# Performance work log

Hardware: AMD Instinct MI355X
Metric: run time of the kernel (lower is better)

The kernel has to match this reference:

```python
import jax, jax.numpy as jnp
import numpy as np

K = 6
EPS = 1e-7
BN_EPS = 1e-5


def tagconv(x, row, col, n, lins, bias, mw1, mb1, bng, bnb, mw2, mb2):
    # gcn_norm: symmetric normalization, no self-loops, edge_weight = 1
    deg = jax.ops.segment_sum(jnp.ones(row.shape[0], x.dtype), col, num_segments=n)
    dis = jnp.where(deg > 0, jax.lax.rsqrt(jnp.maximum(deg, 1.0)), 0.0)
    norm = dis[row] * dis[col]  # [E]
    out = x @ lins[0]
    h = x
    for k in range(1, K + 1):
        # message: relu(edge_weight * x_j) + eps, then scatter-add to destination
        msg = jax.nn.relu(norm[:, None] * h[row]) + EPS  # [E, C]
        h = jax.ops.segment_sum(msg, col, num_segments=n)
        out = out + h @ lins[k]
    out = out + bias
    # MLP: Linear -> BatchNorm1d(eval: running mean 0, var 1) -> ReLU -> Dropout(eval) -> Linear
    z = out @ mw1 + mb1
    z = bng * (z * (1.0 / np.sqrt(1.0 + BN_EPS))) + bnb
    z = jax.nn.relu(z)
    return z @ mw2 + mb2


def setup_inputs() -> dict:
    key = jax.random.key(0)
    ks = jax.random.split(key, 8)
    N, E, F, H, C = 50000, 800000, 128, 128, 64
    s = 0.05
    return {
        "x": jax.random.normal(ks[0], (N, F), jnp.float32),
        "edge_index": jax.random.randint(ks[1], (2, E), 0, N, jnp.int64),
        "lins1": jax.random.normal(ks[2], (K + 1, F, H), jnp.float32) * s,
        "bias1": jnp.zeros((H,), jnp.float32),
        "m1w1": jax.random.normal(ks[3], (H, 2 * H), jnp.float32) * s,
        "m1b1": jnp.zeros((2 * H,), jnp.float32),
        "bn1g": jnp.ones((2 * H,), jnp.float32),
        "bn1b": jnp.zeros((2 * H,), jnp.float32),
        "m1w2": jax.random.normal(ks[4], (2 * H, H), jnp.float32) * s,
        "m1b2": jnp.zeros((H,), jnp.float32),
        "lins2": jax.random.normal(ks[5], (K + 1, H, C), jnp.float32) * s,
        "bias2": jnp.zeros((C,), jnp.float32),
        "m2w1": jax.random.normal(ks[6], (C, 2 * C), jnp.float32) * s,
        "m2b1": jnp.zeros((2 * C,), jnp.float32),
        "bn2g": jnp.ones((2 * C,), jnp.float32),
        "bn2b": jnp.zeros((2 * C,), jnp.float32),
        "m2w2": jax.random.normal(ks[7], (2 * C, C), jnp.float32) * s,
        "m2b2": jnp.zeros((C,), jnp.float32),
    }


def reference(x, edge_index, lins1, bias1, m1w1, m1b1, bn1g, bn1b, m1w2, m1b2,
              lins2, bias2, m2w1, m2b1, bn2g, bn2b, m2w2, m2b2):
    n = x.shape[0]
    row, col = edge_index[0], edge_index[1]
    h = tagconv(x, row, col, n, lins1, bias1, m1w1, m1b1, bn1g, bn1b, m1w2, m1b2)
    h = jax.nn.relu(h)  # dropout is identity in eval mode
    return tagconv(h, row, col, n, lins2, bias2, m2w1, m2b1, bn2g, bn2b, m2w2, m2b2)
```

## Files before the change

kernel.cpp:

```cpp
#include <hip/hip_runtime.h>
#include <hip/hip_bf16.h>


#define EPS_MSG 1e-7f
#define BNSCALE 0.9999950000374997f
#define LO_INV 0.0009765625f

typedef _Float16 half_t;
typedef _Float16 f16x8 __attribute__((ext_vector_type(8)));
typedef float f32x4 __attribute__((ext_vector_type(4)));

__device__ __forceinline__ void gld16(const char* g, char* l) {
    __builtin_amdgcn_global_load_lds(
        (const __attribute__((address_space(1))) void*)g,
        (__attribute__((address_space(3))) void*)l, 16, 0, 0);
}

__device__ __forceinline__ float hlo(unsigned p) {
    unsigned short u = (unsigned short)(p & 0xffffu);
    half_t h;
    __builtin_memcpy(&h, &u, 2);
    return (float)h;
}
__device__ __forceinline__ float hhi(unsigned p) {
    unsigned short u = (unsigned short)(p >> 16);
    half_t h;
    __builtin_memcpy(&h, &u, 2);
    return (float)h;
}
__device__ __forceinline__ unsigned fpack2(float x, float y) {
    half_t a = (half_t)x, b = (half_t)y;
    unsigned short ua, ub;
    __builtin_memcpy(&ua, &a, 2);
    __builtin_memcpy(&ub, &b, 2);
    return (unsigned)ua | ((unsigned)ub << 16);
}

__device__ __forceinline__ float epi_apply(float v, int gc, int epi,
                                           const float* __restrict__ bias,
                                           const float* __restrict__ bng,
                                           const float* __restrict__ bnb) {
    if (epi == 1) {
        v += bias[gc];
    } else if (epi == 2) {
        v = bng[gc] * ((v + bias[gc]) * BNSCALE) + bnb[gc];
        v = fmaxf(v, 0.f);
    } else if (epi == 3) {
        v = fmaxf(v + bias[gc], 0.f);
    }
    return v;
}


__global__ void zero_i32(int* __restrict__ p, int n) {
    int i = blockIdx.x * blockDim.x + threadIdx.x;
    if (i < n) p[i] = 0;
}

__global__ void count_deg(const int* __restrict__ col, int* __restrict__ deg, int E) {
    int e = blockIdx.x * blockDim.x + threadIdx.x;
    if (e < E) atomicAdd(&deg[col[e]], 1);
}

__global__ void compute_dis_s(const int* __restrict__ deg, float* __restrict__ dis,
                              float* __restrict__ s, float* __restrict__ rs, int N) {
    int v = blockIdx.x * blockDim.x + threadIdx.x;
    if (v >= N) return;
    int d = deg[v];
    float di = (d > 0) ? rsqrtf((float)d) : 0.f;
    dis[v] = di;
    s[v] = (d > 0) ? di : 1.f;
    rs[v] = (d > 0) ? sqrtf((float)d) : 1.f;
}

__global__ void scan_blk(const int* __restrict__ deg, int* __restrict__ off,
                         int* __restrict__ bsum, int N) {
    __shared__ int sm[1024];
    int i = blockIdx.x * 1024 + threadIdx.x;
    sm[threadIdx.x] = (i < N) ? deg[i] : 0;
    __syncthreads();
    for (int ofs = 1; ofs < 1024; ofs <<= 1) {
        int t = (threadIdx.x >= (unsigned)ofs) ? sm[threadIdx.x - ofs] : 0;
        __syncthreads();
        sm[threadIdx.x] += t;
        __syncthreads();
    }
    if (i < N) off[i + 1] = sm[threadIdx.x];
    if (threadIdx.x == 0) bsum[blockIdx.x] = sm[1023];
}

__global__ void scan_top(int* __restrict__ bsum, int nb) {
    if (threadIdx.x == 0 && blockIdx.x == 0) {
        int a = 0;
        for (int b = 0; b < nb; ++b) {
            int t = bsum[b];
            bsum[b] = a;
            a += t;
        }
    }
}

__global__ void scan_add(int* __restrict__ off, const int* __restrict__ bsum, int N) {
    int i = blockIdx.x * 1024 + threadIdx.x;
    if (i < N) off[i + 1] += bsum[blockIdx.x];
    if (i == 0) off[0] = 0;
}

__global__ void fill_edges(const int* __restrict__ row, const int* __restrict__ col,
                           const int* __restrict__ off, int* __restrict__ cur,
                           unsigned short* __restrict__ esrc, int E) {
    int e = blockIdx.x * blockDim.x + threadIdx.x;
    if (e >= E) return;
    int c = col[e];
    int pos = off[c] + atomicAdd(&cur[c], 1);
    esrc[pos] = (unsigned short)row[e];
}


__global__ void conv_xg(const float* __restrict__ x, half_t* __restrict__ slab,
                        half_t* __restrict__ g0, const float* __restrict__ dis,
                        const float* __restrict__ s, int total) {
    int i = blockIdx.x * blockDim.x + threadIdx.x;
    if (i >= total) return;
    int v = i >> 7, c = i & 127;
    float xv = x[i];
    slab[(size_t)v * 896 + c] = (half_t)(s[v] * xv);
    g0[i] = (half_t)(dis[v] * fmaxf(xv, 0.f));
}

__device__ __forceinline__ void wcv(const float* __restrict__ in, half_t* __restrict__ oh,
                                    half_t* __restrict__ ol, int nm, int K, int Nn, int i) {
    int KT = nm * K;
    int n = i / KT;
    int rem = i - n * KT;
    int km = rem / K, k = rem - km * K;
    float w = in[(size_t)km * K * Nn + (size_t)k * Nn + n];
    half_t h = (half_t)w;
    oh[i] = h;
    ol[i] = (half_t)((w - (float)h) * 1024.f);
}

__global__ void conv_all(const float* l1, const float* l2, const float* a1, const float* b1,
                         const float* a2, const float* b2, half_t* W1h, half_t* W1l,
                         half_t* W2h, half_t* W2l, half_t* M1ah, half_t* M1al, half_t* M1bh,
                         half_t* M1bl, half_t* M2ah, half_t* M2al, half_t* M2bh,
                         half_t* M2bl) {
    int i = blockIdx.x * blockDim.x + threadIdx.x;
    if (i < 114688) {
        wcv(l1, W1h, W1l, 7, 128, 128, i);
    } else if (i < 172032) {
        int j = i - 114688;
        int np = j >> 7, k = j & 127;
        int km = np >> 6, n = np & 63;
        float w = l2[(size_t)km * 128 * 64 + (size_t)k * 64 + n];
        half_t h = (half_t)w;
        W2h[j] = h;
        W2l[j] = (half_t)((w - (float)h) * 1024.f);
    } else if (i < 204800) {
        wcv(a1, M1ah, M1al, 1, 128, 256, i - 172032);
    } else if (i < 237568) {
        wcv(b1, M1bh, M1bl, 1, 256, 128, i - 204800);
    } else if (i < 245760) {
        wcv(a2, M2ah, M2al, 1, 64, 128, i - 237568);
    } else if (i < 253952) {
        wcv(b2, M2bh, M2bl, 1, 128, 64, i - 245760);
    }
}

__global__ void trows_part(const float* __restrict__ l2, float* __restrict__ partial) {
    __shared__ float sm[256];
    int k = blockIdx.x / 8 + 1;
    int p = blockIdx.x % 8;
    int c = threadIdx.x & 63;
    int q = threadIdx.x >> 6;
    float a = 0.f;
    int kk0 = p * 16 + q * 4;
#pragma unroll
    for (int t = 0; t < 4; ++t)
        a += l2[(size_t)k * 128 * 64 + (kk0 + t) * 64 + c];
    sm[threadIdx.x] = a;
    __syncthreads();
    if (q == 0)
        partial[(size_t)blockIdx.x * 64 + c] =
            (sm[c] + sm[64 + c]) + (sm[128 + c] + sm[192 + c]);
}

__global__ void trows_final(const float* __restrict__ partial, float* __restrict__ T) {
    int j = threadIdx.x >> 6;
    int c = threadIdx.x & 63;
    if (j >= 6) return;
    float a = 0.f;
    for (int k = j + 1; k <= 6; ++k)
#pragma unroll
        for (int p = 0; p < 8; ++p) a += partial[(size_t)((k - 1) * 8 + p) * 64 + c];
    T[j * 64 + c] = a;
}


__global__ void __launch_bounds__(256) prop(const unsigned* __restrict__ gin, int idl,
                                            unsigned* __restrict__ gout, int odl,
                                            const float* __restrict__ dis,
                                            const int* __restrict__ off,
                                            const unsigned short* __restrict__ esrc, int N) {
    const int lane = threadIdx.x & 63;
    const int w = threadIdx.x >> 6;
    const int stride = gridDim.x * 4;
    for (int v = blockIdx.x * 4 + w; v < N; v += stride) {
        int s = off[v], e = off[v + 1];
        float2 A0 = {0.f, 0.f}, A1 = {0.f, 0.f}, A2 = {0.f, 0.f}, A3 = {0.f, 0.f};
        float2 A4 = {0.f, 0.f}, A5 = {0.f, 0.f}, A6 = {0.f, 0.f}, A7 = {0.f, 0.f};
        for (int i = s; i < e; i += 8) {
            unsigned p[8];
            int ok[8];
#pragma unroll
            for (int j = 0; j < 8; ++j) {
                int ij = i + j;
                ok[j] = ij < e;
                int idx = ok[j] ? ij : e - 1;
                p[j] = gin[esrc[idx] * idl + lane];
            }
            A0.x += ok[0] ? hlo(p[0]) : 0.f; A0.y += ok[0] ? hhi(p[0]) : 0.f;
            A1.x += ok[1] ? hlo(p[1]) : 0.f; A1.y += ok[1] ? hhi(p[1]) : 0.f;
            A2.x += ok[2] ? hlo(p[2]) : 0.f; A2.y += ok[2] ? hhi(p[2]) : 0.f;
            A3.x += ok[3] ? hlo(p[3]) : 0.f; A3.y += ok[3] ? hhi(p[3]) : 0.f;
            A4.x += ok[4] ? hlo(p[4]) : 0.f; A4.y += ok[4] ? hhi(p[4]) : 0.f;
            A5.x += ok[5] ? hlo(p[5]) : 0.f; A5.y += ok[5] ? hhi(p[5]) : 0.f;
            A6.x += ok[6] ? hlo(p[6]) : 0.f; A6.y += ok[6] ? hhi(p[6]) : 0.f;
            A7.x += ok[7] ? hlo(p[7]) : 0.f; A7.y += ok[7] ? hhi(p[7]) : 0.f;
        }
        float ax = ((A0.x + A1.x) + (A2.x + A3.x)) + ((A4.x + A5.x) + (A6.x + A7.x));
        float ay = ((A0.y + A1.y) + (A2.y + A3.y)) + ((A4.y + A5.y) + (A6.y + A7.y));
        float dv = dis[v];
        float ce = (float)(e - s) * EPS_MSG;
        float hx = fmaf(dv, ax, ce);
        float hy = fmaf(dv, ay, ce);
        gout[v * odl + lane] = fpack2(dv * hx, dv * hy);
    }
}


template <int FINAL>
__global__ void __launch_bounds__(256) prop64(
    const half_t* __restrict__ uin, int ldu, const half_t* __restrict__ pj, int ldp,
    half_t* __restrict__ uout, int ldo, const float* __restrict__ dis,
    const int* __restrict__ off, const unsigned short* __restrict__ esrc,
    const float* __restrict__ tj, const float* __restrict__ bias2, int N) {
    const int c = threadIdx.x & 63;
    const int w = threadIdx.x >> 6;
    const int stride = gridDim.x * 4;
    for (int v = blockIdx.x * 4 + w; v < N; v += stride) {
        int s = off[v], e = off[v + 1];
        float a0 = 0.f, a1 = 0.f, a2 = 0.f, a3 = 0.f;
        float a4 = 0.f, a5 = 0.f, a6 = 0.f, a7 = 0.f;
        for (int i = s; i < e; i += 8) {
            float q[8];
            int ok[8];
#pragma unroll
            for (int j = 0; j < 8; ++j) {
                int ij = i + j;
                ok[j] = ij < e;
                int idx = ok[j] ? ij : e - 1;
                q[j] = (float)uin[(size_t)esrc[idx] * ldu + c];
            }
            a0 += ok[0] ? q[0] : 0.f;
            a1 += ok[1] ? q[1] : 0.f;
            a2 += ok[2] ? q[2] : 0.f;
            a3 += ok[3] ? q[3] : 0.f;
            a4 += ok[4] ? q[4] : 0.f;
            a5 += ok[5] ? q[5] : 0.f;
            a6 += ok[6] ? q[6] : 0.f;
            a7 += ok[7] ? q[7] : 0.f;
        }
        float acc = ((a0 + a1) + (a2 + a3)) + ((a4 + a5) + (a6 + a7));
        float dv = dis[v];
        float base = (float)pj[(size_t)v * ldp + c] + (float)(e - s) * EPS_MSG * tj[c];
        float u = fmaf(dv, acc, base);
        if (FINAL)
            uout[(size_t)v * ldo + c] = (half_t)(u + bias2[c]);
        else
            uout[(size_t)v * ldo + c] = (half_t)(dv * u);
    }
}


__global__ __launch_bounds__(512) void gemmc(
    int M, int kiters, const half_t* __restrict__ A, int lda,
    const half_t* __restrict__ Bhp, const half_t* __restrict__ Blp, int ldb,
    half_t* __restrict__ Cp, int ldc, const float* __restrict__ rs,
    const float* __restrict__ bias) {
    constexpr int ABY = 8192, BBY = 8192, BUFBY = ABY + 2 * BBY;
    __shared__ __align__(16) char lds[2][BUFBY];

    const int tid = threadIdx.x, lane = tid & 63, w = tid >> 6;
    const int wr = w >> 1, wc = w & 1;
    const int m0 = blockIdx.x * 128;
    const int l15 = lane & 15, lq = lane >> 4;
    const int lr = lane >> 2, lc = lane & 3;

    const char* gA = (const char*)A;
    const char* gBh = (const char*)Bhp;
    const char* gBl = (const char*)Blp;
    const size_t ldaB = (size_t)lda * 2, ldbB = (size_t)ldb * 2;

    auto stage = [&](int kt, int buf) {
        const int k0b = kt * 64;
        char* base = lds[0] + buf * BUFBY;
        int r = w * 16 + lr;
        int sc = (lc ^ (r & 3)) << 4;
        {
            int gv = m0 + r;
            if (gv >= M) gv = M - 1;
            gld16(gA + (size_t)gv * ldaB + k0b + sc, base + w * 1024);
        }
        {
            size_t goff = (size_t)r * ldbB + k0b + sc;
            gld16(gBh + goff, base + ABY + w * 1024);
            gld16(gBl + goff, base + ABY + BBY + w * 1024);
        }
    };

    f32x4 acch[2][4], accl[2][4];
#pragma unroll
    for (int fm = 0; fm < 2; ++fm)
#pragma unroll
        for (int fn = 0; fn < 4; ++fn) {
            acch[fm][fn] = (f32x4){0.f, 0.f, 0.f, 0.f};
            accl[fm][fn] = (f32x4){0.f, 0.f, 0.f, 0.f};
        }

    auto compute = [&](int buf) {
        const char* Ab = lds[0] + buf * BUFBY;
        const char* Bhb = Ab + ABY;
        const char* Blb = Ab + ABY + BBY;
        f16x8 af[2];
#pragma unroll
        for (int fm = 0; fm < 2; ++fm) {
            int ra = wr * 32 + fm * 16 + l15;
            af[fm] = *(const f16x8*)(Ab + ra * 64 + ((lq ^ (ra & 3)) << 4));
        }
#pragma unroll
        for (int fn = 0; fn < 4; ++fn) {
            int rb = wc * 64 + fn * 16 + l15;
            int o = rb * 64 + ((lq ^ (rb & 3)) << 4);
            f16x8 bhv = *(const f16x8*)(Bhb + o);
            f16x8 blv = *(const f16x8*)(Blb + o);
#pragma unroll
            for (int fm = 0; fm < 2; ++fm) {
                acch[fm][fn] = __builtin_amdgcn_mfma_f32_16x16x32_f16(af[fm], bhv, acch[fm][fn], 0, 0, 0);
                accl[fm][fn] = __builtin_amdgcn_mfma_f32_16x16x32_f16(af[fm], blv, accl[fm][fn], 0, 0, 0);
            }
        }
    };

    stage(0, 0);
    int buf = 0;
    for (int kt = 0; kt < kiters; ++kt) {
        __syncthreads();
        if (kt + 1 < kiters) stage(kt + 1, buf ^ 1);
        compute(buf);
        buf ^= 1;
    }

#pragma unroll
    for (int fm = 0; fm < 2; ++fm)
#pragma unroll
        for (int fn = 0; fn < 4; ++fn)
#pragma unroll
            for (int i = 0; i < 4; ++i) {
                int gr = m0 + wr * 32 + fm * 16 + lq * 4 + i;
                if (gr >= M) continue;
                int gc = wc * 64 + fn * 16 + l15;
                float v = acch[fm][fn][i] + accl[fm][fn][i] * LO_INV;
                v = v * rs[gr] + bias[gc];
                Cp[(size_t)gr * ldc + gc] = (half_t)v;
            }
}


template <int KT, int NS, int OUTF32>
__global__ __launch_bounds__(256) void gemmn(
    int M, const half_t* __restrict__ A, int lda, const half_t* __restrict__ Bhp,
    const half_t* __restrict__ Blp, int ldb, void* __restrict__ Cp, int ldc, int epi,
    const float* __restrict__ bias, const float* __restrict__ bng,
    const float* __restrict__ bnb, const float* __restrict__ scaleRows, int scaleStrip) {
    constexpr int KI = KT / 32;
    constexpr int T = NS * KI;
    constexpr int CPR = KT / 8;
    constexpr int LPR = CPR;
    constexpr int RPC = 64 / LPR;
    constexpr int SW = (CPR < 16) ? CPR - 1 : 15;
    constexpr int ACH = (64 * KT * 2) / 1024;
    constexpr int ACW = ACH / 4;
    constexpr int ABY = 64 * KT * 2;
    constexpr int BPB = 4096;
    __shared__ __align__(16) char lds[ABY + 4 * BPB];

    const int tid = threadIdx.x, lane = tid & 63, w = tid >> 6;
    const int m0 = blockIdx.x * 64;
    const int l15 = lane & 15, lq = lane >> 4;
    const int lr = lane >> 2, lc = lane & 3;

    const char* gA = (const char*)A;
    const char* gBh = (const char*)Bhp;
    const char* gBl = (const char*)Blp;
    const size_t ldaB = (size_t)lda * 2, ldbB = (size_t)ldb * 2;

#pragma unroll
    for (int i = 0; i < ACW; ++i) {
        int c = w * ACW + i;
        int r = c * RPC + lane / LPR;
        int col = lane % LPR;
        int scol = col ^ (r & SW);
        int gv = m0 + r;
        if (gv >= M) gv = M - 1;
        gld16(gA + (size_t)gv * ldaB + scol * 16, lds + c * 1024);
    }

    auto stageB = [&](int ns, int kt, int buf) {
        char* bb = lds + ABY + buf * 2 * BPB;
        int r = w * 16 + lr;
        int sc = (lc ^ (r & 3)) << 4;
        size_t goff = (size_t)(ns * 64 + r) * ldbB + kt * 64 + sc;
        gld16(gBh + goff, bb + w * 1024);
        gld16(gBl + goff, bb + BPB + w * 1024);
    };

    f32x4 acch[4], accl[4];

    auto compute = [&](int buf, int kt) {
        const char* Ab = lds;
        const char* Bhb = lds + ABY + buf * 2 * BPB;
        const char* Blb = Bhb + BPB;
        int ra = w * 16 + l15;
        int cc = kt * 4 + lq;
        f16x8 af = *(const f16x8*)(Ab + ra * (KT * 2) + ((cc ^ (ra & SW)) << 4));
#pragma unroll
        for (int fn = 0; fn < 4; ++fn) {
            int rb = fn * 16 + l15;
            int o = rb * 64 + ((lq ^ (rb & 3)) << 4);
            f16x8 bhv = *(const f16x8*)(Bhb + o);
            f16x8 blv = *(const f16x8*)(Blb + o);
            acch[fn] = __builtin_amdgcn_mfma_f32_16x16x32_f16(af, bhv, acch[fn], 0, 0, 0);
            accl[fn] = __builtin_amdgcn_mfma_f32_16x16x32_f16(af, blv, accl[fn], 0, 0, 0);
        }
    };

    stageB(0, 0, 0);
    int buf = 0;
    for (int t = 0; t < T; ++t) {
        int ns = t / KI, kt = t - ns * KI;
        __syncthreads();
        if (t + 1 < T) {
            int t1 = t + 1;
            stageB(t1 / KI, t1 - (t1 / KI) * KI, buf ^ 1);
        }
        if (kt == 0) {
#pragma unroll
            for (int fn = 0; fn < 4; ++fn) {
                acch[fn] = (f32x4){0.f, 0.f, 0.f, 0.f};
                accl[fn] = (f32x4){0.f, 0.f, 0.f, 0.f};
            }
        }
        compute(buf, kt);
        if (kt == KI - 1) {
#pragma unroll
            for (int fn = 0; fn < 4; ++fn)
#pragma unroll
                for (int i = 0; i < 4; ++i) {
                    int gr = m0 + w * 16 + lq * 4 + i;
                    if (gr >= M) continue;
                    int gc = ns * 64 + fn * 16 + l15;
                    float v = acch[fn][i] + accl[fn][i] * LO_INV;
                    if (ns == scaleStrip) v *= scaleRows[gr];
                    v = epi_apply(v, gc, epi, bias, bng, bnb);
                    if (OUTF32)
                        ((float*)Cp)[(size_t)gr * ldc + gc] = v;
                    else
                        ((half_t*)Cp)[(size_t)gr * ldc + gc] = (half_t)v;
                }
        }
        buf ^= 1;
    }
}

extern "C" void kernel_launch(void* const* d_in, const int* in_sizes, int n_in,
                              void* d_out, int out_size, void* d_ws, size_t ws_size,
                              hipStream_t stream) {
    const float* x     = (const float*)d_in[0];
    const int*   ei    = (const int*)d_in[1];
    const float* lins1 = (const float*)d_in[2];
    const float* bias1 = (const float*)d_in[3];
    const float* m1w1  = (const float*)d_in[4];
    const float* m1b1  = (const float*)d_in[5];
    const float* bn1g  = (const float*)d_in[6];
    const float* bn1b  = (const float*)d_in[7];
    const float* m1w2  = (const float*)d_in[8];
    const float* m1b2  = (const float*)d_in[9];
    const float* lins2 = (const float*)d_in[10];
    const float* bias2 = (const float*)d_in[11];
    const float* m2w1  = (const float*)d_in[12];
    const float* m2b1  = (const float*)d_in[13];
    const float* bn2g  = (const float*)d_in[14];
    const float* bn2b  = (const float*)d_in[15];
    const float* m2w2  = (const float*)d_in[16];
    const float* m2b2  = (const float*)d_in[17];
    float* out = (float*)d_out;

    const int N = in_sizes[0] / 128;
    const int E = in_sizes[1] / 2;
    const int* row = ei;
    const int* col = ei + E;

    char* ws = (char*)d_ws;
    size_t o = 0;
    auto alloc = [&](size_t bytes) {
        void* p = ws + o;
        o += (bytes + 255) & ~(size_t)255;
        return p;
    };
    int*            deg  = (int*)alloc((size_t)N * 4);
    int*            cur  = (int*)alloc((size_t)N * 4);
    float*          dis  = (float*)alloc((size_t)N * 4);
    float*          sA   = (float*)alloc((size_t)N * 4);
    float*          rsA  = (float*)alloc((size_t)N * 4);
    int*            off  = (int*)alloc((size_t)(N + 1) * 4);
    int*            bsum = (int*)alloc(1024 * 4);
    float*          Trow = (float*)alloc(6 * 64 * 4);
    float*          Tpar = (float*)alloc(48 * 64 * 4);
    unsigned short* esrc = (unsigned short*)alloc((size_t)E * 2);
    half_t* g0    = (half_t*)alloc((size_t)N * 128 * 2);
    half_t* ACC   = (half_t*)alloc((size_t)N * 128 * 2);
    half_t* Z     = (half_t*)alloc((size_t)N * 256 * 2);
    half_t* H1    = (half_t*)alloc((size_t)N * 128 * 2);
    half_t* ACC2  = (half_t*)alloc((size_t)N * 64 * 2);
    half_t* Wc1h  = (half_t*)alloc((size_t)128 * 896 * 2);
    half_t* Wc1l  = (half_t*)alloc((size_t)128 * 896 * 2);
    half_t* Wc2h  = (half_t*)alloc((size_t)448 * 128 * 2);
    half_t* Wc2l  = (half_t*)alloc((size_t)448 * 128 * 2);
    half_t* Wm1ah = (half_t*)alloc((size_t)256 * 128 * 2);
    half_t* Wm1al = (half_t*)alloc((size_t)256 * 128 * 2);
    half_t* Wm1bh = (half_t*)alloc((size_t)128 * 256 * 2);
    half_t* Wm1bl = (half_t*)alloc((size_t)128 * 256 * 2);
    half_t* Wm2ah = (half_t*)alloc((size_t)128 * 64 * 2);
    half_t* Wm2al = (half_t*)alloc((size_t)128 * 64 * 2);
    half_t* Wm2bh = (half_t*)alloc((size_t)64 * 128 * 2);
    half_t* Wm2bl = (half_t*)alloc((size_t)64 * 128 * 2);
    half_t* slab  = (half_t*)alloc((size_t)N * 896 * 2);
    (void)ws_size;

    const int TPB = 256;
    const int nb = (N + 1023) / 1024;
    zero_i32<<<(N + TPB - 1) / TPB, TPB, 0, stream>>>(deg, N);
    zero_i32<<<(N + TPB - 1) / TPB, TPB, 0, stream>>>(cur, N);
    count_deg<<<(E + TPB - 1) / TPB, TPB, 0, stream>>>(col, deg, E);
    compute_dis_s<<<(N + TPB - 1) / TPB, TPB, 0, stream>>>(deg, dis, sA, rsA, N);
    scan_blk<<<nb, 1024, 0, stream>>>(deg, off, bsum, N);
    scan_top<<<1, 64, 0, stream>>>(bsum, nb);
    scan_add<<<nb, 1024, 0, stream>>>(off, bsum, N);
    fill_edges<<<(E + TPB - 1) / TPB, TPB, 0, stream>>>(row, col, off, cur, esrc, E);
    conv_all<<<(253952 + TPB - 1) / TPB, TPB, 0, stream>>>(
        lins1, lins2, m1w1, m1w2, m2w1, m2w2, Wc1h, Wc1l, Wc2h, Wc2l, Wm1ah, Wm1al, Wm1bh,
        Wm1bl, Wm2ah, Wm2al, Wm2bh, Wm2bl);
    trows_part<<<48, 256, 0, stream>>>(lins2, Tpar);
    trows_final<<<1, 384, 0, stream>>>(Tpar, Trow);
    conv_xg<<<(N * 128 + TPB - 1) / TPB, TPB, 0, stream>>>(x, slab, g0, dis, sA, N * 128);

    unsigned* slabU = (unsigned*)slab;
    unsigned* g0U = (unsigned*)g0;
    const int HG = (N + 63) / 64;
    const int HG128 = (N + 127) / 128;

    prop<<<2048, 256, 0, stream>>>(g0U, 64, slabU + 64, 448, dis, off, esrc, N);
    for (int k = 2; k <= 6; ++k)
        prop<<<2048, 256, 0, stream>>>(slabU + (size_t)(k - 1) * 64, 448,
                                       slabU + (size_t)k * 64, 448, dis, off, esrc, N);
    gemmc<<<HG128, 512, 0, stream>>>(N, 28, slab, 896, Wc1h, Wc1l, 896, ACC, 128, rsA, bias1);
    gemmn<128, 4, 0><<<HG, 256, 0, stream>>>(
        N, ACC, 128, Wm1ah, Wm1al, 128, Z, 256, 2, m1b1, bn1g, bn1b, nullptr, -1);
    gemmn<256, 2, 0><<<HG, 256, 0, stream>>>(
        N, Z, 256, Wm1bh, Wm1bl, 256, H1, 128, 3, m1b2, nullptr, nullptr, nullptr, -1);

    gemmn<128, 7, 0><<<HG, 256, 0, stream>>>(
        N, H1, 128, Wc2h, Wc2l, 128, slab, 448, 0, nullptr, nullptr, nullptr, dis, 6);

    half_t* ub0 = g0;
    half_t* ub1 = g0 + (size_t)N * 64;
    prop64<0><<<2048, 256, 0, stream>>>(slab + 384, 448, slab + 320, 448, ub0, 64, dis, off,
                                        esrc, Trow + 5 * 64, nullptr, N);
    prop64<0><<<2048, 256, 0, stream>>>(ub0, 64, slab + 256, 448, ub1, 64, dis, off, esrc,
                                        Trow + 4 * 64, nullptr, N);
    prop64<0><<<2048, 256, 0, stream>>>(ub1, 64, slab + 192, 448, ub0, 64, dis, off, esrc,
                                        Trow + 3 * 64, nullptr, N);
    prop64<0><<<2048, 256, 0, stream>>>(ub0, 64, slab + 128, 448, ub1, 64, dis, off, esrc,
                                        Trow + 2 * 64, nullptr, N);
    prop64<0><<<2048, 256, 0, stream>>>(ub1, 64, slab + 64, 448, ub0, 64, dis, off, esrc,
                                        Trow + 1 * 64, nullptr, N);
    prop64<1><<<2048, 256, 0, stream>>>(ub0, 64, slab, 448, ACC2, 64, dis, off, esrc,
                                        Trow + 0 * 64, bias2, N);

    gemmn<64, 2, 0><<<HG, 256, 0, stream>>>(
        N, ACC2, 64, Wm2ah, Wm2al, 64, Z, 128, 2, m2b1, bn2g, bn2b, nullptr, -1);
    gemmn<128, 1, 1><<<HG, 256, 0, stream>>>(
        N, Z, 128, Wm2bh, Wm2bl, 128, out, 64, 1, m2b2, nullptr, nullptr, nullptr, -1);
}
```

Measured before the change: 673.3 us.

## Fuse MLP GEMM chains into single kernels keeping intermediates in LDS

Merges the three back-to-back GEMMs after the first conv (MLP linear+BN+ReLU, second linear+ReLU, and the projection by lins2) into one kernel, and likewise the two MLP GEMMs at the end. Intermediate activations (Z, H1) live in shared memory instead of round-tripping through global memory, and several launches are dropped. It also merges the two zeroing kernels into one. In exchange, the larger per-block LDS footprint (about 64KB for fuse1) may lower occupancy and limit latency hiding.

Result: no change. 674.9 us (+0.2%).

```diff
diff --git a/kernel.cpp b/kernel.cpp
--- a/kernel.cpp
+++ b/kernel.cpp
@@ -36,25 +36,13 @@
     return (unsigned)ua | ((unsigned)ub << 16);
 }
 
-__device__ __forceinline__ float epi_apply(float v, int gc, int epi,
-                                           const float* __restrict__ bias,
-                                           const float* __restrict__ bng,
-                                           const float* __restrict__ bnb) {
-    if (epi == 1) {
-        v += bias[gc];
-    } else if (epi == 2) {
-        v = bng[gc] * ((v + bias[gc]) * BNSCALE) + bnb[gc];
-        v = fmaxf(v, 0.f);
-    } else if (epi == 3) {
-        v = fmaxf(v + bias[gc], 0.f);
-    }
-    return v;
-}
-
-
-__global__ void zero_i32(int* __restrict__ p, int n) {
+
+__global__ void zero2_i32(int* __restrict__ a, int* __restrict__ b, int n) {
     int i = blockIdx.x * blockDim.x + threadIdx.x;
-    if (i < n) p[i] = 0;
+    if (i < n) {
+        a[i] = 0;
+        b[i] = 0;
+    }
 }
 
 __global__ void count_deg(const int* __restrict__ col, int* __restrict__ deg, int E) {
@@ -377,63 +365,70 @@
 }
 
 
-template <int KT, int NS, int OUTF32>
-__global__ __launch_bounds__(256) void gemmn(
-    int M, const half_t* __restrict__ A, int lda, const half_t* __restrict__ Bhp,
-    const half_t* __restrict__ Blp, int ldb, void* __restrict__ Cp, int ldc, int epi,
-    const float* __restrict__ bias, const float* __restrict__ bng,
-    const float* __restrict__ bnb, const float* __restrict__ scaleRows, int scaleStrip) {
-    constexpr int KI = KT / 32;
-    constexpr int T = NS * KI;
-    constexpr int CPR = KT / 8;
-    constexpr int LPR = CPR;
-    constexpr int RPC = 64 / LPR;
-    constexpr int SW = (CPR < 16) ? CPR - 1 : 15;
-    constexpr int ACH = (64 * KT * 2) / 1024;
-    constexpr int ACW = ACH / 4;
-    constexpr int ABY = 64 * KT * 2;
+__global__ __launch_bounds__(256) void fuse1(
+    int M, const half_t* __restrict__ ACC, const half_t* __restrict__ W1h,
+    const half_t* __restrict__ W1l, const half_t* __restrict__ W2h,
+    const half_t* __restrict__ W2l, const half_t* __restrict__ WPh,
+    const half_t* __restrict__ WPl, half_t* __restrict__ P, int ldp,
+    const float* __restrict__ b1, const float* __restrict__ bg,
+    const float* __restrict__ bb, const float* __restrict__ b2,
+    const float* __restrict__ disArr) {
     constexpr int BPB = 4096;
-    __shared__ __align__(16) char lds[ABY + 4 * BPB];
+    __shared__ __align__(16) char ldsA[16384];
+    __shared__ __align__(16) char ldsZ[32768];
+    __shared__ __align__(16) char ldsB[4 * BPB];
 
     const int tid = threadIdx.x, lane = tid & 63, w = tid >> 6;
     const int m0 = blockIdx.x * 64;
     const int l15 = lane & 15, lq = lane >> 4;
     const int lr = lane >> 2, lc = lane & 3;
 
-    const char* gA = (const char*)A;
-    const char* gBh = (const char*)Bhp;
-    const char* gBl = (const char*)Blp;
-    const size_t ldaB = (size_t)lda * 2, ldbB = (size_t)ldb * 2;
-
-#pragma unroll
-    for (int i = 0; i < ACW; ++i) {
-        int c = w * ACW + i;
-        int r = c * RPC + lane / LPR;
-        int col = lane % LPR;
-        int scol = col ^ (r & SW);
+#pragma unroll
+    for (int i = 0; i < 4; ++i) {
+        int c = w * 4 + i;
+        int r = c * 4 + (lane >> 4);
+        int colx = lane & 15;
+        int scol = colx ^ (r & 15);
         int gv = m0 + r;
         if (gv >= M) gv = M - 1;
-        gld16(gA + (size_t)gv * ldaB + scol * 16, lds + c * 1024);
-    }
-
-    auto stageB = [&](int ns, int kt, int buf) {
-        char* bb = lds + ABY + buf * 2 * BPB;
+        gld16((const char*)ACC + (size_t)gv * 256 + scol * 16, ldsA + c * 1024);
+    }
+
+    auto stageB = [&](const char* Bh_, const char* Bl_, size_t ldbB_, int rowoff, int kt,
+                      int bufb) {
+        char* bbuf = ldsB + bufb * 2 * BPB;
         int r = w * 16 + lr;
         int sc = (lc ^ (r & 3)) << 4;
-        size_t goff = (size_t)(ns * 64 + r) * ldbB + kt * 64 + sc;
-        gld16(gBh + goff, bb + w * 1024);
-        gld16(gBl + goff, bb + BPB + w * 1024);
+        size_t goff = (size_t)(rowoff + r) * ldbB_ + (size_t)kt * 64 + sc;
+        gld16(Bh_ + goff, bbuf + w * 1024);
+        gld16(Bl_ + goff, bbuf + BPB + w * 1024);
+    };
+    auto stageTile = [&](int t, int bufb) {
+        if (t < 16) {
+            stageB((const char*)W1h, (const char*)W1l, 256, (t >> 2) * 64, t & 3, bufb);
+        } else if (t < 32) {
+            int tt = t - 16;
+            stageB((const char*)W2h, (const char*)W2l, 512, (tt >> 3) * 64, tt & 7, bufb);
+        } else {
+            int tt = t - 32;
+            stageB((const char*)WPh, (const char*)WPl, 256, (tt >> 2) * 64, tt & 3, bufb);
+        }
     };
 
     f32x4 acch[4], accl[4];
-
-    auto compute = [&](int buf, int kt) {
-        const char* Ab = lds;
-        const char* Bhb = lds + ABY + buf * 2 * BPB;
+    auto zacc = [&]() {
+#pragma unroll
+        for (int fn = 0; fn < 4; ++fn) {
+            acch[fn] = (f32x4){0.f, 0.f, 0.f, 0.f};
+            accl[fn] = (f32x4){0.f, 0.f, 0.f, 0.f};
+        }
+    };
+    auto computeT = [&](const char* Ab, int astride, int asw, int bufb, int cc0) {
+        const char* Bhb = ldsB + bufb * 2 * BPB;
         const char* Blb = Bhb + BPB;
         int ra = w * 16 + l15;
-        int cc = kt * 4 + lq;
-        f16x8 af = *(const f16x8*)(Ab + ra * (KT * 2) + ((cc ^ (ra & SW)) << 4));
+        int cc = cc0 + lq;
+        f16x8 af = *(const f16x8*)(Ab + ra * astride + ((cc ^ (ra & asw)) << 4));
 #pragma unroll
         for (int fn = 0; fn < 4; ++fn) {
             int rb = fn * 16 + l15;
@@ -445,39 +440,176 @@
         }
     };
 
-    stageB(0, 0, 0);
+    stageTile(0, 0);
     int buf = 0;
-    for (int t = 0; t < T; ++t) {
-        int ns = t / KI, kt = t - ns * KI;
+    for (int t = 0; t < 60; ++t) {
         __syncthreads();
-        if (t + 1 < T) {
-            int t1 = t + 1;
-            stageB(t1 / KI, t1 - (t1 / KI) * KI, buf ^ 1);
-        }
-        if (kt == 0) {
-#pragma unroll
-            for (int fn = 0; fn < 4; ++fn) {
-                acch[fn] = (f32x4){0.f, 0.f, 0.f, 0.f};
-                accl[fn] = (f32x4){0.f, 0.f, 0.f, 0.f};
-            }
-        }
-        compute(buf, kt);
-        if (kt == KI - 1) {
-#pragma unroll
-            for (int fn = 0; fn < 4; ++fn)
-#pragma unroll
-                for (int i = 0; i < 4; ++i) {
-                    int gr = m0 + w * 16 + lq * 4 + i;
-                    if (gr >= M) continue;
-                    int gc = ns * 64 + fn * 16 + l15;
-                    float v = acch[fn][i] + accl[fn][i] * LO_INV;
-                    if (ns == scaleStrip) v *= scaleRows[gr];
-                    v = epi_apply(v, gc, epi, bias, bng, bnb);
-                    if (OUTF32)
-                        ((float*)Cp)[(size_t)gr * ldc + gc] = v;
-                    else
-                        ((half_t*)Cp)[(size_t)gr * ldc + gc] = (half_t)v;
-                }
+        if (t + 1 < 60) stageTile(t + 1, buf ^ 1);
+        if (t < 16) {
+            int kt = t & 3, ns = t >> 2;
+            if (kt == 0) zacc();
+            computeT(ldsA, 256, 15, buf, kt * 4);
+            if (kt == 3) {
+#pragma unroll
+                for (int fn = 0; fn < 4; ++fn)
+#pragma unroll
+                    for (int i = 0; i < 4; ++i) {
+                        int r = w * 16 + lq * 4 + i;
+                        int gc = ns * 64 + fn * 16 + l15;
+                        float v = acch[fn][i] + accl[fn][i] * LO_INV;
+                        v = bg[gc] * ((v + b1[gc]) * BNSCALE) + bb[gc];
+                        v = fmaxf(v, 0.f);
+                        int ch = (gc >> 3) ^ (r & 15);
+                        *(half_t*)(ldsZ + r * 512 + (ch << 4) + (gc & 7) * 2) = (half_t)v;
+                    }
+            }
+        } else if (t < 32) {
+            int tt = t - 16, kt = tt & 7, ns = tt >> 3;
+            if (kt == 0) zacc();
+            computeT(ldsZ, 512, 15, buf, kt * 4);
+            if (kt == 7) {
+#pragma unroll
+                for (int fn = 0; fn < 4; ++fn)
+#pragma unroll
+                    for (int i = 0; i < 4; ++i) {
+                        int r = w * 16 + lq * 4 + i;
+                        int gc = ns * 64 + fn * 16 + l15;
+                        float v = acch[fn][i] + accl[fn][i] * LO_INV;
+                        v = fmaxf(v + b2[gc], 0.f);
+                        int ch = (gc >> 3) ^ (r & 15);
+                        *(half_t*)(ldsA + r * 256 + (ch << 4) + (gc & 7) * 2) = (half_t)v;
+                    }
+            }
+        } else {
+            int tt = t - 32, kt = tt & 3, ns = tt >> 2;
+            if (kt == 0) zacc();
+            computeT(ldsA, 256, 15, buf, kt * 4);
+            if (kt == 3) {
+#pragma unroll
+                for (int fn = 0; fn < 4; ++fn)
+#pragma unroll
+                    for (int i = 0; i < 4; ++i) {
+                        int gr = m0 + w * 16 + lq * 4 + i;
+                        if (gr >= M) continue;
+                        int gc = ns * 64 + fn * 16 + l15;
+                        float v = acch[fn][i] + accl[fn][i] * LO_INV;
+                        if (ns == 6) v *= disArr[gr];
+                        P[(size_t)gr * ldp + gc] = (half_t)v;
+                    }
+            }
+        }
+        buf ^= 1;
+    }
+}
+
+
+__global__ __launch_bounds__(256) void fuse2(
+    int M, const half_t* __restrict__ ACC2, const half_t* __restrict__ W1h,
+    const half_t* __restrict__ W1l, const half_t* __restrict__ W2h,
+    const half_t* __restrict__ W2l, float* __restrict__ outp,
+    const float* __restrict__ b1, const float* __restrict__ bg,
+    const float* __restrict__ bb, const float* __restrict__ b2) {
+    constexpr int BPB = 4096;
+    __shared__ __align__(16) char ldsA[8192];
+    __shared__ __align__(16) char ldsZ[16384];
+    __shared__ __align__(16) char ldsB[4 * BPB];
+
+    const int tid = threadIdx.x, lane = tid & 63, w = tid >> 6;
+    const int m0 = blockIdx.x * 64;
+    const int l15 = lane & 15, lq = lane >> 4;
+    const int lr = lane >> 2, lc = lane & 3;
+
+#pragma unroll
+    for (int i = 0; i < 2; ++i) {
+        int c = w * 2 + i;
+        int r = c * 8 + (lane >> 3);
+        int colx = lane & 7;
+        int scol = colx ^ (r & 7);
+        int gv = m0 + r;
+        if (gv >= M) gv = M - 1;
+        gld16((const char*)ACC2 + (size_t)gv * 128 + scol * 16, ldsA + c * 1024);
+    }
+
+    auto stageB = [&](const char* Bh_, const char* Bl_, size_t ldbB_, int rowoff, int kt,
+                      int bufb) {
+        char* bbuf = ldsB + bufb * 2 * BPB;
+        int r = w * 16 + lr;
+        int sc = (lc ^ (r & 3)) << 4;
+        size_t goff = (size_t)(rowoff + r) * ldbB_ + (size_t)kt * 64 + sc;
+        gld16(Bh_ + goff, bbuf + w * 1024);
+        gld16(Bl_ + goff, bbuf + BPB + w * 1024);
+    };
+    auto stageTile = [&](int t, int bufb) {
+        if (t < 4)
+            stageB((const char*)W1h, (const char*)W1l, 128, (t >> 1) * 64, t & 1, bufb);
+        else
+            stageB((const char*)W2h, (const char*)W2l, 256, 0, t - 4, bufb);
+    };
+
+    f32x4 acch[4], accl[4];
+    auto zacc = [&]() {
+#pragma unroll
+        for (int fn = 0; fn < 4; ++fn) {
+            acch[fn] = (f32x4){0.f, 0.f, 0.f, 0.f};
+            accl[fn] = (f32x4){0.f, 0.f, 0.f, 0.f};
+        }
+    };
+    auto computeT = [&](const char* Ab, int astride, int asw, int bufb, int cc0) {
+        const char* Bhb = ldsB + bufb * 2 * BPB;
+        const char* Blb = Bhb + BPB;
+        int ra = w * 16 + l15;
+        int cc = cc0 + lq;
+        f16x8 af = *(const f16x8*)(Ab + ra * astride + ((cc ^ (ra & asw)) << 4));
+#pragma unroll
+        for (int fn = 0; fn < 4; ++fn) {
+            int rb = fn * 16 + l15;
+            int o = rb * 64 + ((lq ^ (rb & 3)) << 4);
+            f16x8 bhv = *(const f16x8*)(Bhb + o);
+            f16x8 blv = *(const f16x8*)(Blb + o);
+            acch[fn] = __builtin_amdgcn_mfma_f32_16x16x32_f16(af, bhv, acch[fn], 0, 0, 0);
+            accl[fn] = __builtin_amdgcn_mfma_f32_16x16x32_f16(af, blv, accl[fn], 0, 0, 0);
+        }
+    };
+
+    stageTile(0, 0);
+    int buf = 0;
+    for (int t = 0; t < 8; ++t) {
+        __syncthreads();
+        if (t + 1 < 8) stageTile(t + 1, buf ^ 1);
+        if (t < 4) {
+            int kt = t & 1, ns = t >> 1;
+            if (kt == 0) zacc();
+            computeT(ldsA, 128, 7, buf, kt * 4);
+            if (kt == 1) {
+#pragma unroll
+                for (int fn = 0; fn < 4; ++fn)
+#pragma unroll
+                    for (int i = 0; i < 4; ++i) {
+                        int r = w * 16 + lq * 4 + i;
+                        int gc = ns * 64 + fn * 16 + l15;
+                        float v = acch[fn][i] + accl[fn][i] * LO_INV;
+                        v = bg[gc] * ((v + b1[gc]) * BNSCALE) + bb[gc];
+                        v = fmaxf(v, 0.f);
+                        int ch = (gc >> 3) ^ (r & 15);
+                        *(half_t*)(ldsZ + r * 256 + (ch << 4) + (gc & 7) * 2) = (half_t)v;
+                    }
+            }
+        } else {
+            int tt = t - 4;
+            if (tt == 0) zacc();
+            computeT(ldsZ, 256, 15, buf, tt * 4);
+            if (tt == 3) {
+#pragma unroll
+                for (int fn = 0; fn < 4; ++fn)
+#pragma unroll
+                    for (int i = 0; i < 4; ++i) {
+                        int gr = m0 + w * 16 + lq * 4 + i;
+                        if (gr >= M) continue;
+                        int gc = fn * 16 + l15;
+                        float v = acch[fn][i] + accl[fn][i] * LO_INV;
+                        outp[(size_t)gr * 64 + gc] = v + b2[gc];
+                    }
+            }
         }
         buf ^= 1;
     }
@@ -530,8 +662,6 @@
     unsigned short* esrc = (unsigned short*)alloc((size_t)E * 2);
     half_t* g0    = (half_t*)alloc((size_t)N * 128 * 2);
     half_t* ACC   = (half_t*)alloc((size_t)N * 128 * 2);
-    half_t* Z     = (half_t*)alloc((size_t)N * 256 * 2);
-    half_t* H1    = (half_t*)alloc((size_t)N * 128 * 2);
     half_t* ACC2  = (half_t*)alloc((size_t)N * 64 * 2);
     half_t* Wc1h  = (half_t*)alloc((size_t)128 * 896 * 2);
     half_t* Wc1l  = (half_t*)alloc((size_t)128 * 896 * 2);
@@ -550,8 +680,7 @@
 
     const int TPB = 256;
     const int nb = (N + 1023) / 1024;
-    zero_i32<<<(N + TPB - 1) / TPB, TPB, 0, stream>>>(deg, N);
-    zero_i32<<<(N + TPB - 1) / TPB, TPB, 0, stream>>>(cur, N);
+    zero2_i32<<<(N + TPB - 1) / TPB, TPB, 0, stream>>>(deg, cur, N);
     count_deg<<<(E + TPB - 1) / TPB, TPB, 0, stream>>>(col, deg, E);
     compute_dis_s<<<(N + TPB - 1) / TPB, TPB, 0, stream>>>(deg, dis, sA, rsA, N);
     scan_blk<<<nb, 1024, 0, stream>>>(deg, off, bsum, N);
@@ -575,13 +704,9 @@
         prop<<<2048, 256, 0, stream>>>(slabU + (size_t)(k - 1) * 64, 448,
                                        slabU + (size_t)k * 64, 448, dis, off, esrc, N);
     gemmc<<<HG128, 512, 0, stream>>>(N, 28, slab, 896, Wc1h, Wc1l, 896, ACC, 128, rsA, bias1);
-    gemmn<128, 4, 0><<<HG, 256, 0, stream>>>(
-        N, ACC, 128, Wm1ah, Wm1al, 128, Z, 256, 2, m1b1, bn1g, bn1b, nullptr, -1);
-    gemmn<256, 2, 0><<<HG, 256, 0, stream>>>(
-        N, Z, 256, Wm1bh, Wm1bl, 256, H1, 128, 3, m1b2, nullptr, nullptr, nullptr, -1);
-
-    gemmn<128, 7, 0><<<HG, 256, 0, stream>>>(
-        N, H1, 128, Wc2h, Wc2l, 128, slab, 448, 0, nullptr, nullptr, nullptr, dis, 6);
+
+    fuse1<<<HG, 256, 0, stream>>>(N, ACC, Wm1ah, Wm1al, Wm1bh, Wm1bl, Wc2h, Wc2l, slab, 448,
+                                  m1b1, bn1g, bn1b, m1b2, dis);
 
     half_t* ub0 = g0;
     half_t* ub1 = g0 + (size_t)N * 64;
@@ -598,8 +723,6 @@
     prop64<1><<<2048, 256, 0, stream>>>(ub0, 64, slab, 448, ACC2, 64, dis, off, esrc,
                                         Trow + 0 * 64, bias2, N);
 
-    gemmn<64, 2, 0><<<HG, 256, 0, stream>>>(
-        N, ACC2, 64, Wm2ah, Wm2al, 64, Z, 128, 2, m2b1, bn2g, bn2b, nullptr, -1);
-    gemmn<128, 1, 1><<<HG, 256, 0, stream>>>(
-        N, Z, 128, Wm2bh, Wm2bl, 128, out, 64, 1, m2b2, nullptr, nullptr, nullptr, -1);
-}
+    fuse2<<<HG, 256, 0, stream>>>(N, ACC2, Wm2ah, Wm2al, Wm2bh, Wm2bl, out, m2b1, bn2g, bn2b,
+                                  m2b2);
+}
```

## Merge propagation hops into cooperative kernels and fuse final MLP GEMMs

Applied to the files above, without the earlier changes.

Replaces the six layer-1 propagation launches and the six Horner propagation launches with two cooperative kernels that step through the hops using grid-wide syncs. It also fuses the final two MLP GEMMs into one kernel that keeps the hidden activations in LDS, and merges the two zeroing kernels into one. The intent is to cut launch overhead and the round trip of the Z intermediate through global memory. In exchange the cooperative grid is limited to 1024 blocks, down from 2048, which may reduce latency hiding in the gather loops, and each grid.sync adds barrier cost.

Result: slower. 1.992 ms (+195.8%).

```diff
diff --git a/kernel.cpp b/kernel.cpp
--- a/kernel.cpp
+++ b/kernel.cpp
@@ -1,5 +1,6 @@
 #include <hip/hip_runtime.h>
 #include <hip/hip_bf16.h>
+#include <hip/hip_cooperative_groups.h>
 
 
 #define EPS_MSG 1e-7f
@@ -9,6 +10,8 @@
 typedef _Float16 half_t;
 typedef _Float16 f16x8 __attribute__((ext_vector_type(8)));
 typedef float f32x4 __attribute__((ext_vector_type(4)));
+
+namespace cg = cooperative_groups;
 
 __device__ __forceinline__ void gld16(const char* g, char* l) {
     __builtin_amdgcn_global_load_lds(
@@ -52,9 +55,12 @@
 }
 
 
-__global__ void zero_i32(int* __restrict__ p, int n) {
+__global__ void zero2_i32(int* __restrict__ a, int* __restrict__ b, int n) {
     int i = blockIdx.x * blockDim.x + threadIdx.x;
-    if (i < n) p[i] = 0;
+    if (i < n) {
+        a[i] = 0;
+        b[i] = 0;
+    }
 }
 
 __global__ void count_deg(const int* __restrict__ col, int* __restrict__ deg, int E) {
@@ -197,11 +203,11 @@
 }
 
 
-__global__ void __launch_bounds__(256) prop(const unsigned* __restrict__ gin, int idl,
-                                            unsigned* __restrict__ gout, int odl,
-                                            const float* __restrict__ dis,
-                                            const int* __restrict__ off,
-                                            const unsigned short* __restrict__ esrc, int N) {
+__device__ __forceinline__ void prop_hop(const unsigned* __restrict__ gin, int idl,
+                                         unsigned* __restrict__ gout, int odl,
+                                         const float* __restrict__ dis,
+                                         const int* __restrict__ off,
+                                         const unsigned short* __restrict__ esrc, int N) {
     const int lane = threadIdx.x & 63;
     const int w = threadIdx.x >> 6;
     const int stride = gridDim.x * 4;
@@ -238,13 +244,29 @@
     }
 }
 
-
-template <int FINAL>
-__global__ void __launch_bounds__(256) prop64(
-    const half_t* __restrict__ uin, int ldu, const half_t* __restrict__ pj, int ldp,
-    half_t* __restrict__ uout, int ldo, const float* __restrict__ dis,
-    const int* __restrict__ off, const unsigned short* __restrict__ esrc,
-    const float* __restrict__ tj, const float* __restrict__ bias2, int N) {
+__global__ void __launch_bounds__(256) prop6(const unsigned* __restrict__ g0U,
+                                             unsigned* __restrict__ slabU,
+                                             const float* __restrict__ dis,
+                                             const int* __restrict__ off,
+                                             const unsigned short* __restrict__ esrc, int N) {
+    cg::grid_group grid = cg::this_grid();
+    prop_hop(g0U, 64, slabU + 64, 448, dis, off, esrc, N);
+    for (int k = 2; k <= 6; ++k) {
+        grid.sync();
+        prop_hop(slabU + (size_t)(k - 1) * 64, 448, slabU + (size_t)k * 64, 448, dis, off,
+                 esrc, N);
+    }
+}
+
+__device__ __forceinline__ void horner_step(const half_t* __restrict__ uin, int ldu,
+                                            const half_t* __restrict__ pj,
+                                            half_t* __restrict__ uout,
+                                            const float* __restrict__ dis,
+                                            const int* __restrict__ off,
+                                            const unsigned short* __restrict__ esrc,
+                                            const float* __restrict__ tj,
+                                            const float* __restrict__ bias2, int finalStep,
+                                            int N) {
     const int c = threadIdx.x & 63;
     const int w = threadIdx.x >> 6;
     const int stride = gridDim.x * 4;
@@ -273,13 +295,36 @@
         }
         float acc = ((a0 + a1) + (a2 + a3)) + ((a4 + a5) + (a6 + a7));
         float dv = dis[v];
-        float base = (float)pj[(size_t)v * ldp + c] + (float)(e - s) * EPS_MSG * tj[c];
+        float base = (float)pj[(size_t)v * 448 + c] + (float)(e - s) * EPS_MSG * tj[c];
         float u = fmaf(dv, acc, base);
-        if (FINAL)
-            uout[(size_t)v * ldo + c] = (half_t)(u + bias2[c]);
+        if (finalStep)
+            uout[(size_t)v * 64 + c] = (half_t)(u + bias2[c]);
         else
-            uout[(size_t)v * ldo + c] = (half_t)(dv * u);
-    }
+            uout[(size_t)v * 64 + c] = (half_t)(dv * u);
+    }
+}
+
+__global__ void __launch_bounds__(256) horner6(const half_t* __restrict__ slab,
+                                               half_t* __restrict__ ub0,
+                                               half_t* __restrict__ ub1,
+                                               half_t* __restrict__ ACC2,
+                                               const float* __restrict__ dis,
+                                               const int* __restrict__ off,
+                                               const unsigned short* __restrict__ esrc,
+                                               const float* __restrict__ Trow,
+                                               const float* __restrict__ bias2, int N) {
+    cg::grid_group grid = cg::this_grid();
+    horner_step(slab + 384, 448, slab + 320, ub0, dis, off, esrc, Trow + 5 * 64, nullptr, 0, N);
+    grid.sync();
+    horner_step(ub0, 64, slab + 256, ub1, dis, off, esrc, Trow + 4 * 64, nullptr, 0, N);
+    grid.sync();
+    horner_step(ub1, 64, slab + 192, ub0, dis, off, esrc, Trow + 3 * 64, nullptr, 0, N);
+    grid.sync();
+    horner_step(ub0, 64, slab + 128, ub1, dis, off, esrc, Trow + 2 * 64, nullptr, 0, N);
+    grid.sync();
+    horner_step(ub1, 64, slab + 64, ub0, dis, off, esrc, Trow + 1 * 64, nullptr, 0, N);
+    grid.sync();
+    horner_step(ub0, 64, slab, ACC2, dis, off, esrc, Trow, bias2, 1, N);
 }
 
 
@@ -478,6 +523,119 @@
                     else
                         ((half_t*)Cp)[(size_t)gr * ldc + gc] = (half_t)v;
                 }
+        }
+        buf ^= 1;
+    }
+}
+
+
+__global__ __launch_bounds__(256) void fuse2(
+    int M, const half_t* __restrict__ ACC2, const half_t* __restrict__ W1h,
+    const half_t* __restrict__ W1l, const half_t* __restrict__ W2h,
+    const half_t* __restrict__ W2l, float* __restrict__ outp,
+    const float* __restrict__ b1, const float* __restrict__ bg,
+    const float* __restrict__ bb, const float* __restrict__ b2) {
+    constexpr int BPB = 4096;
+    __shared__ __align__(16) char ldsA[8192];
+    __shared__ __align__(16) char ldsZ[16384];
+    __shared__ __align__(16) char ldsB[4 * BPB];
+
+    const int tid = threadIdx.x, lane = tid & 63, w = tid >> 6;
+    const int m0 = blockIdx.x * 64;
+    const int l15 = lane & 15, lq = lane >> 4;
+    const int lr = lane >> 2, lc = lane & 3;
+
+#pragma unroll
+    for (int i = 0; i < 2; ++i) {
+        int c = w * 2 + i;
+        int r = c * 8 + (lane >> 3);
+        int colx = lane & 7;
+        int scol = colx ^ (r & 7);
+        int gv = m0 + r;
+        if (gv >= M) gv = M - 1;
+        gld16((const char*)ACC2 + (size_t)gv * 128 + scol * 16, ldsA + c * 1024);
+    }
+
+    auto stageB = [&](const char* Bh_, const char* Bl_, size_t ldbB_, int rowoff, int kt,
+                      int bufb) {
+        char* bbuf = ldsB + bufb * 2 * BPB;
+        int r = w * 16 + lr;
+        int sc = (lc ^ (r & 3)) << 4;
+        size_t goff = (size_t)(rowoff + r) * ldbB_ + (size_t)kt * 64 + sc;
+        gld16(Bh_ + goff, bbuf + w * 1024);
+        gld16(Bl_ + goff, bbuf + BPB + w * 1024);
+    };
+    auto stageTile = [&](int t, int bufb) {
+        if (t < 4)
+            stageB((const char*)W1h, (const char*)W1l, 128, (t >> 1) * 64, t & 1, bufb);
+        else
+            stageB((const char*)W2h, (const char*)W2l, 256, 0, t - 4, bufb);
+    };
+
+    f32x4 acch[4], accl[4];
+    auto zacc = [&]() {
+#pragma unroll
+        for (int fn = 0; fn < 4; ++fn) {
+            acch[fn] = (f32x4){0.f, 0.f, 0.f, 0.f};
+            accl[fn] = (f32x4){0.f, 0.f, 0.f, 0.f};
+        }
+    };
+    auto computeT = [&](const char* Ab, int astride, int asw, int bufb, int cc0) {
+        const char* Bhb = ldsB + bufb * 2 * BPB;
+        const char* Blb = Bhb + BPB;
+        int ra = w * 16 + l15;
+        int cc = cc0 + lq;
+        f16x8 af = *(const f16x8*)(Ab + ra * astride + ((cc ^ (ra & asw)) << 4));
+#pragma unroll
+        for (int fn = 0; fn < 4; ++fn) {
+            int rb = fn * 16 + l15;
+            int o = rb * 64 + ((lq ^ (rb & 3)) << 4);
+            f16x8 bhv = *(const f16x8*)(Bhb + o);
+            f16x8 blv = *(const f16x8*)(Blb + o);
+            acch[fn] = __builtin_amdgcn_mfma_f32_16x16x32_f16(af, bhv, acch[fn], 0, 0, 0);
+            accl[fn] = __builtin_amdgcn_mfma_f32_16x16x32_f16(af, blv, accl[fn], 0, 0, 0);
+        }
+    };
+
+    stageTile(0, 0);
+    int buf = 0;
+    for (int t = 0; t < 8; ++t) {
+        __syncthreads();
+        if (t + 1 < 8) stageTile(t + 1, buf ^ 1);
+        if (t < 4) {
+            int kt = t & 1, ns = t >> 1;
+            if (kt == 0) zacc();
+            computeT(ldsA, 128, 7, buf, kt * 4);
+            if (kt == 1) {
+#pragma unroll
+                for (int fn = 0; fn < 4; ++fn)
+#pragma unroll
+                    for (int i = 0; i < 4; ++i) {
+                        int r = w * 16 + lq * 4 + i;
+                        int gc = ns * 64 + fn * 16 + l15;
+                        float v = acch[fn][i] + accl[fn][i] * LO_INV;
+                        v = bg[gc] * ((v + b1[gc]) * BNSCALE) + bb[gc];
+                        v = fmaxf(v, 0.f);
+                        int ch = (gc >> 3) ^ (r & 15);
+                        *(half_t*)(ldsZ + r * 256 + (ch << 4) + (gc & 7) * 2) = (half_t)v;
+                    }
+            }
+        } else {
+            int tt = t - 4;
+            if (tt == 0) zacc();
+            computeT(ldsZ, 256, 15, buf, tt * 4);
+            if (tt == 3) {
+#pragma unroll
+                for (int fn = 0; fn < 4; ++fn)
+#pragma unroll
+                    for (int i = 0; i < 4; ++i) {
+                        int gr = m0 + w * 16 + lq * 4 + i;
+                        if (gr >= M) continue;
+                        int gc = fn * 16 + l15;
+                        float v = acch[fn][i] + accl[fn][i] * LO_INV;
+                        outp[(size_t)gr * 64 + gc] = v + b2[gc];
+                    }
+            }
         }
         buf ^= 1;
     }
@@ -550,8 +708,7 @@
 
     const int TPB = 256;
     const int nb = (N + 1023) / 1024;
-    zero_i32<<<(N + TPB - 1) / TPB, TPB, 0, stream>>>(deg, N);
-    zero_i32<<<(N + TPB - 1) / TPB, TPB, 0, stream>>>(cur, N);
+    zero2_i32<<<(N + TPB - 1) / TPB, TPB, 0, stream>>>(deg, cur, N);
     count_deg<<<(E + TPB - 1) / TPB, TPB, 0, stream>>>(col, deg, E);
     compute_dis_s<<<(N + TPB - 1) / TPB, TPB, 0, stream>>>(deg, dis, sA, rsA, N);
     scan_blk<<<nb, 1024, 0, stream>>>(deg, off, bsum, N);
@@ -570,36 +727,40 @@
     const int HG = (N + 63) / 64;
     const int HG128 = (N + 127) / 128;
 
-    prop<<<2048, 256, 0, stream>>>(g0U, 64, slabU + 64, 448, dis, off, esrc, N);
-    for (int k = 2; k <= 6; ++k)
-        prop<<<2048, 256, 0, stream>>>(slabU + (size_t)(k - 1) * 64, 448,
-                                       slabU + (size_t)k * 64, 448, dis, off, esrc, N);
+    {
+        const unsigned* a0 = g0U;
+        unsigned* a1 = slabU;
+        const float* a2 = dis;
+        const int* a3 = off;
+        const unsigned short* a4 = esrc;
+        int a5 = N;
+        void* args[] = {&a0, &a1, &a2, &a3, &a4, &a5};
+        hipLaunchCooperativeKernel((void*)prop6, dim3(1024), dim3(256), args, 0, stream);
+    }
     gemmc<<<HG128, 512, 0, stream>>>(N, 28, slab, 896, Wc1h, Wc1l, 896, ACC, 128, rsA, bias1);
+
     gemmn<128, 4, 0><<<HG, 256, 0, stream>>>(
         N, ACC, 128, Wm1ah, Wm1al, 128, Z, 256, 2, m1b1, bn1g, bn1b, nullptr, -1);
     gemmn<256, 2, 0><<<HG, 256, 0, stream>>>(
         N, Z, 256, Wm1bh, Wm1bl, 256, H1, 128, 3, m1b2, nullptr, nullptr, nullptr, -1);
-
     gemmn<128, 7, 0><<<HG, 256, 0, stream>>>(
         N, H1, 128, Wc2h, Wc2l, 128, slab, 448, 0, nullptr, nullptr, nullptr, dis, 6);
 
-    half_t* ub0 = g0;
-    half_t* ub1 = g0 + (size_t)N * 64;
-    prop64<0><<<2048, 256, 0, stream>>>(slab + 384, 448, slab + 320, 448, ub0, 64, dis, off,
-                                        esrc, Trow + 5 * 64, nullptr, N);
-    prop64<0><<<2048, 256, 0, stream>>>(ub0, 64, slab + 256, 448, ub1, 64, dis, off, esrc,
-                                        Trow + 4 * 64, nullptr, N);
-    prop64<0><<<2048, 256, 0, stream>>>(ub1, 64, slab + 192, 448, ub0, 64, dis, off, esrc,
-                                        Trow + 3 * 64, nullptr, N);
-    prop64<0><<<2048, 256, 0, stream>>>(ub0, 64, slab + 128, 448, ub1, 64, dis, off, esrc,
-                                        Trow + 2 * 64, nullptr, N);
-    prop64<0><<<2048, 256, 0, stream>>>(ub1, 64, slab + 64, 448, ub0, 64, dis, off, esrc,
-                                        Trow + 1 * 64, nullptr, N);
-    prop64<1><<<2048, 256, 0, stream>>>(ub0, 64, slab, 448, ACC2, 64, dis, off, esrc,
-                                        Trow + 0 * 64, bias2, N);
-
-    gemmn<64, 2, 0><<<HG, 256, 0, stream>>>(
-        N, ACC2, 64, Wm2ah, Wm2al, 64, Z, 128, 2, m2b1, bn2g, bn2b, nullptr, -1);
-    gemmn<128, 1, 1><<<HG, 256, 0, stream>>>(
-        N, Z, 128, Wm2bh, Wm2bl, 128, out, 64, 1, m2b2, nullptr, nullptr, nullptr, -1);
-}
+    {
+        const half_t* a0 = slab;
+        half_t* a1 = g0;
+        half_t* a2 = g0 + (size_t)N * 64;
+        half_t* a3 = ACC2;
+        const float* a4 = dis;
+        const int* a5 = off;
+        const unsigned short* a6 = esrc;
+        const float* a7 = Trow;
+        const float* a8 = bias2;
+        int a9 = N;
+        void* args[] = {&a0, &a1, &a2, &a3, &a4, &a5, &a6, &a7, &a8, &a9};
+        hipLaunchCooperativeKernel((void*)horner6, dim3(1024), dim3(256), args, 0, stream);
+    }
+
+    fuse2<<<HG, 256, 0, stream>>>(N, ACC2, Wm2ah, Wm2al, Wm2bh, Wm2bl, out, m2b1, bn2g, bn2b,
+                                  m2b2);
+}
```
